# Kernel tuning notes

Hardware: AMD Instinct MI355X
Metric: run time of the kernel (lower is better)

## Reference

```python
import jax, jax.numpy as jnp
import numpy as np

DIM = 1024
NUM_HEADS = 16
SEQ_LEN = 4096


def setup_inputs() -> dict:
    key = jax.random.key(0)
    ks = jax.random.split(key, 9)
    s = DIM ** -0.5  # typical init scale for weights
    return {
        "x": jax.random.normal(ks[0], (SEQ_LEN, DIM), dtype=jnp.float32),
        "Wq": jax.random.normal(ks[1], (DIM, DIM), dtype=jnp.float32) * s,
        "bq": jax.random.normal(ks[2], (DIM,), dtype=jnp.float32) * s,
        "Wk": jax.random.normal(ks[3], (DIM, DIM), dtype=jnp.float32) * s,
        "bk": jax.random.normal(ks[4], (DIM,), dtype=jnp.float32) * s,
        "Wv": jax.random.normal(ks[5], (DIM, DIM), dtype=jnp.float32) * s,
        "bv": jax.random.normal(ks[6], (DIM,), dtype=jnp.float32) * s,
        "Wp": jax.random.normal(ks[7], (DIM, DIM), dtype=jnp.float32) * s,
        "bp": jax.random.normal(ks[8], (DIM,), dtype=jnp.float32) * s,
    }


def reference(x, Wq, bq, Wk, bk, Wv, bv, Wp, bp):
    T, C = x.shape
    H = NUM_HEADS
    Dh = C // H
    # QKV projections (eqx.nn.Linear: y = W @ x + b, vmapped over tokens)
    q = (x @ Wq.T + bq).reshape(T, H, Dh).swapaxes(0, 1)  # [H, T, Dh]
    k = (x @ Wk.T + bk).reshape(T, H, Dh).swapaxes(0, 1)
    v = (x @ Wv.T + bv).reshape(T, H, Dh).swapaxes(0, 1)
    # NOTE: original scales by C**-0.5 (full dim), not head_dim**-0.5
    attn = jnp.einsum("htd,hsd->hts", q, k) * (C ** -0.5)  # [H, T, T]
    causal = jnp.tril(jnp.ones((T, T), dtype=bool))[None, :, :]
    attn = jnp.where(causal, attn, -jnp.inf)
    attn = jax.nn.softmax(attn, axis=-1)
    out = jnp.einsum("hts,hsd->htd", attn, v)  # [H, T, Dh]
    out = out.swapaxes(0, 1).reshape(T, C)
    return out @ Wp.T + bp
```

## Files before the change

kernel.cpp:

```cpp
#include <hip/hip_runtime.h>
#include <stdint.h>

typedef unsigned short u16;
typedef __bf16 bf16x8 __attribute__((ext_vector_type(8)));
typedef u16 u16x8 __attribute__((ext_vector_type(8)));
typedef float f32x4 __attribute__((ext_vector_type(4)));
typedef float f32x16 __attribute__((ext_vector_type(16)));

#define SEQ 4096
#define CD 1024
#define NH 16
#define DHD 64

__device__ __forceinline__ u16 f2bf(float f) {
  union { float f; unsigned u; } v; v.f = f;
  unsigned r = v.u + 0x7fffu + ((v.u >> 16) & 1u);
  return (u16)(r >> 16);
}
__device__ __forceinline__ u16 f2bf_trunc(float f) {
  union { float f; unsigned u; } v; v.f = f;
  return (u16)(v.u >> 16);
}

__device__ __forceinline__ void load_lds16(const u16* g, u16* l) {
  __builtin_amdgcn_global_load_lds((const __attribute__((address_space(1))) void*)g,
                                   (__attribute__((address_space(3))) void*)l, 16, 0, 0);
}

__global__ __launch_bounds__(256) void cvt_all(const float* __restrict__ x, const float* __restrict__ Wq,
                                               const float* __restrict__ Wk, const float* __restrict__ Wv,
                                               const float* __restrict__ Wp,
                                               u16* __restrict__ xb, u16* __restrict__ Wb, u16* __restrict__ Wpb) {
  int b = blockIdx.x;
  const float* src; u16* dst; int base;
  if (b < 2048)      { src = x;  dst = xb;             base = b; }
  else if (b < 2560) { src = Wq; dst = Wb;             base = b - 2048; }
  else if (b < 3072) { src = Wk; dst = Wb + CD * CD;   base = b - 2560; }
  else if (b < 3584) { src = Wv; dst = Wb + 2*CD*CD;   base = b - 3072; }
  else               { src = Wp; dst = Wpb;            base = b - 3584; }
  int i = (base * 256 + (int)threadIdx.x) * 8;
  float4 a = *(const float4*)(src + i);
  float4 c = *(const float4*)(src + i + 4);
  u16x8 o;
  o[0] = f2bf(a.x); o[1] = f2bf(a.y); o[2] = f2bf(a.z); o[3] = f2bf(a.w);
  o[4] = f2bf(c.x); o[5] = f2bf(c.y); o[6] = f2bf(c.z); o[7] = f2bf(c.w);
  *(u16x8*)(dst + i) = o;
}

template<int MODE>
__device__ __forceinline__ void gemm_core(const u16* __restrict__ A, const u16* __restrict__ Bw,
                                          const float* __restrict__ bias, void* __restrict__ outp,
                                          float oscale) {
  constexpr int K = CD, N = CD;
  __shared__ u16 As[128 * 32];
  __shared__ u16 Bs[128 * 32];
  const int tid = threadIdx.x;
  const int w = tid >> 6, L = tid & 63, q = L >> 4, ln = L & 15;
  const int rowA0 = blockIdx.y * 128, rowB0 = blockIdx.x * 128;
  const int wr = (w >> 1) * 64, wc = (w & 1) * 64;
  f32x4 acc[4][4] = {};
  for (int k0 = 0; k0 < K; k0 += 32) {
#pragma unroll
    for (int pass = 0; pass < 2; ++pass) {
      int off = pass * 4096 + tid * 16;
      int row = off >> 6;
      int cole = (off & 63) >> 1;
      load_lds16(A + (size_t)(rowA0 + row) * K + k0 + cole, As + pass * 2048 + w * 512);
      load_lds16(Bw + (size_t)(rowB0 + row) * K + k0 + cole, Bs + pass * 2048 + w * 512);
    }
    __syncthreads();
    bf16x8 af[4], bg[4];
#pragma unroll
    for (int i = 0; i < 4; ++i) af[i] = *(const bf16x8*)(As + (wr + i * 16 + ln) * 32 + q * 8);
#pragma unroll
    for (int i = 0; i < 4; ++i) bg[i] = *(const bf16x8*)(Bs + (wc + i * 16 + ln) * 32 + q * 8);
#pragma unroll
    for (int i = 0; i < 4; ++i)
#pragma unroll
      for (int j = 0; j < 4; ++j)
        acc[i][j] = __builtin_amdgcn_mfma_f32_16x16x32_bf16(af[i], bg[j], acc[i][j], 0, 0, 0);
    __syncthreads();
  }
#pragma unroll
  for (int i = 0; i < 4; ++i) {
#pragma unroll
    for (int j = 0; j < 4; ++j) {
      int col = rowB0 + wc + j * 16 + ln;
      float bb = bias[col];
#pragma unroll
      for (int r = 0; r < 4; ++r) {
        int row = rowA0 + wr + i * 16 + q * 4 + r;
        float v = (acc[i][j][r] + bb) * oscale;
        if (MODE == 0)      ((u16*)outp)[(size_t)row * N + col] = f2bf(v);
        else if (MODE == 1) ((u16*)outp)[(size_t)col * SEQ + row] = f2bf(v);
        else                ((float*)outp)[(size_t)row * N + col] = v;
      }
    }
  }
}

__global__ __launch_bounds__(256) void gemm_qkv(const u16* __restrict__ A, const u16* __restrict__ W3,
                                                const float* __restrict__ bq, const float* __restrict__ bk,
                                                const float* __restrict__ bv, u16* __restrict__ Qb,
                                                u16* __restrict__ Kb, u16* __restrict__ VTb) {
  int z = blockIdx.z;
  if (z == 0)      gemm_core<0>(A, W3,              bq, Qb,  0.03125f);
  else if (z == 1) gemm_core<0>(A, W3 + CD * CD,    bk, Kb,  1.0f);
  else             gemm_core<1>(A, W3 + 2 * CD * CD, bv, VTb, 1.0f);
}

__global__ __launch_bounds__(256) void gemm_proj(const u16* __restrict__ A, const u16* __restrict__ Bw,
                                                 const float* __restrict__ bias, float* __restrict__ out) {
  gemm_core<2>(A, Bw, bias, out, 1.0f);
}

__global__ __launch_bounds__(256, 3) void attn_kernel(const u16* __restrict__ Q, const u16* __restrict__ Kg,
                                                      const u16* __restrict__ VTg, u16* __restrict__ O) {
  __shared__ u16 Ks[64 * 72];
  __shared__ u16 Vt[64 * 72];
  __shared__ u16 Ps[4 * 32 * 72];
  const int tid = threadIdx.x, w = tid >> 6, L = tid & 63;
  const int ln = L & 31, hh = L >> 5;
  const int b = blockIdx.x;
  const int qb = (SEQ / 128 - 1) - (b >> 4);
  const int h = b & 15;
  const int qbase = qb * 128;
  const int colH = h * DHD;
  const int qrow0 = qbase + w * 32;
  bf16x8 qf[4];
#pragma unroll
  for (int kk = 0; kk < 4; ++kk)
    qf[kk] = *(const bf16x8*)(Q + (size_t)(qrow0 + ln) * CD + colH + kk * 16 + hh * 8);
  f32x16 o_acc[2] = {};
  float lsum[16] = {};
  u16* Pw = Ps + w * 32 * 72;
  const int ntiles = 2 * qb + 2;
  const int row0 = tid >> 3, row1 = 32 + (tid >> 3), x0 = tid & 7;
  u16x8 kr[2], vr[2];
  kr[0] = *(const u16x8*)(Kg + (size_t)row0 * CD + colH + x0 * 8);
  kr[1] = *(const u16x8*)(Kg + (size_t)row1 * CD + colH + x0 * 8);
  vr[0] = *(const u16x8*)(VTg + (size_t)(colH + row0) * SEQ + x0 * 8);
  vr[1] = *(const u16x8*)(VTg + (size_t)(colH + row1) * SEQ + x0 * 8);
  for (int jt = 0; jt < ntiles; ++jt) {
    __syncthreads();
    *(u16x8*)(Ks + row0 * 72 + x0 * 8) = kr[0];
    *(u16x8*)(Ks + row1 * 72 + x0 * 8) = kr[1];
    *(u16x8*)(Vt + row0 * 72 + x0 * 8) = vr[0];
    *(u16x8*)(Vt + row1 * 72 + x0 * 8) = vr[1];
    __syncthreads();
    if (jt + 1 < ntiles) {
      size_t kb2 = (size_t)(jt + 1) * 64;
      kr[0] = *(const u16x8*)(Kg + (kb2 + row0) * CD + colH + x0 * 8);
      kr[1] = *(const u16x8*)(Kg + (kb2 + row1) * CD + colH + x0 * 8);
      vr[0] = *(const u16x8*)(VTg + (size_t)(colH + row0) * SEQ + kb2 + x0 * 8);
      vr[1] = *(const u16x8*)(VTg + (size_t)(colH + row1) * SEQ + kb2 + x0 * 8);
    }
    const int kbase = jt * 64;
    if (kbase <= qrow0 + 31) {
      const bool diag = (kbase + 63 > qrow0);
#pragma unroll
      for (int nt = 0; nt < 2; ++nt) {
        f32x16 acc = {};
#pragma unroll
        for (int kk = 0; kk < 4; ++kk) {
          bf16x8 kf = *(const bf16x8*)(Ks + (nt * 32 + ln) * 72 + kk * 16 + hh * 8);
          acc = __builtin_amdgcn_mfma_f32_32x32x16_bf16(qf[kk], kf, acc, 0, 0, 0);
        }
        const int kg = kbase + nt * 32 + ln;
#pragma unroll
        for (int r = 0; r < 16; ++r) {
          const int rrow = (r & 3) + 8 * (r >> 2) + 4 * hh;
          float sv = acc[r];
          if (diag && kg > qrow0 + rrow) sv = -1e30f;
          float p = __expf(sv);
          lsum[r] += p;
          Pw[rrow * 72 + nt * 32 + ln] = f2bf_trunc(p);
        }
      }
      asm volatile("s_waitcnt lgkmcnt(0)" ::: "memory");
      bf16x8 pf[4];
#pragma unroll
      for (int kk = 0; kk < 4; ++kk)
        pf[kk] = *(const bf16x8*)(Pw + ln * 72 + kk * 16 + hh * 8);
#pragma unroll
      for (int nt = 0; nt < 2; ++nt)
#pragma unroll
        for (int kk = 0; kk < 4; ++kk) {
          bf16x8 vf = *(const bf16x8*)(Vt + (nt * 32 + ln) * 72 + kk * 16 + hh * 8);
          o_acc[nt] = __builtin_amdgcn_mfma_f32_32x32x16_bf16(pf[kk], vf, o_acc[nt], 0, 0, 0);
        }
    }
  }
#pragma unroll
  for (int m = 1; m < 32; m <<= 1)
#pragma unroll
    for (int r = 0; r < 16; ++r) lsum[r] += __shfl_xor(lsum[r], m, 64);
  float inv[16];
#pragma unroll
  for (int r = 0; r < 16; ++r) inv[r] = 1.0f / lsum[r];
#pragma unroll
  for (int nt = 0; nt < 2; ++nt)
#pragma unroll
    for (int r = 0; r < 16; ++r) {
      const int rrow = (r & 3) + 8 * (r >> 2) + 4 * hh;
      const int row = qrow0 + rrow;
      const int col = colH + nt * 32 + ln;
      O[(size_t)row * CD + col] = f2bf(o_acc[nt][r] * inv[r]);
    }
}

extern "C" void kernel_launch(void* const* d_in, const int* in_sizes, int n_in,
                              void* d_out, int out_size, void* d_ws, size_t ws_size,
                              hipStream_t stream) {
  const float* x  = (const float*)d_in[0];
  const float* Wq = (const float*)d_in[1];
  const float* bq = (const float*)d_in[2];
  const float* Wk = (const float*)d_in[3];
  const float* bk = (const float*)d_in[4];
  const float* Wv = (const float*)d_in[5];
  const float* bv = (const float*)d_in[6];
  const float* Wp = (const float*)d_in[7];
  const float* bp = (const float*)d_in[8];

  char* ws = (char*)d_ws;
  u16* xb  = (u16*)(ws);
  u16* Wb  = (u16*)(ws + (8u << 20));
  u16* Wpb = (u16*)(ws + (14u << 20));
  u16* Qb  = (u16*)(ws + (16u << 20));
  u16* Kb  = (u16*)(ws + (24u << 20));
  u16* VTb = (u16*)(ws + (32u << 20));
  u16* Ab  = (u16*)(ws + (40u << 20));

  cvt_all<<<4096, 256, 0, stream>>>(x, Wq, Wk, Wv, Wp, xb, Wb, Wpb);
  gemm_qkv<<<dim3(CD / 128, SEQ / 128, 3), 256, 0, stream>>>(xb, Wb, bq, bk, bv, Qb, Kb, VTb);
  attn_kernel<<<(SEQ / 128) * NH, 256, 0, stream>>>(Qb, Kb, VTb, Ab);
  gemm_proj<<<dim3(CD / 128, SEQ / 128), 256, 0, stream>>>(Ab, Wpb, bp, (float*)d_out);
}
```

Baseline: 242.6 us.

## Keep attention probabilities in registers via transposed MFMA and permlane swap

Restructures the attention kernel to compute S^T (keys x queries), so each lane owns one query row. The P tile is then packed to bf16 in registers and redistributed with v_permlane32_swap rather than going through LDS. The block shrinks to 128 threads and 64 query rows, and K/V tiles are double-buffered so each iteration needs one barrier instead of two. Row sums collapse to a single scalar per lane, and outputs are written as 4-wide vectors. Smaller blocks double the grid but reduce K/V reuse per block, and the permlane instruction ties the code to newer CDNA targets.

```diff
diff --git a/kernel.cpp b/kernel.cpp
--- a/kernel.cpp
+++ b/kernel.cpp
@@ -4,6 +4,7 @@
 typedef unsigned short u16;
 typedef __bf16 bf16x8 __attribute__((ext_vector_type(8)));
 typedef u16 u16x8 __attribute__((ext_vector_type(8)));
+typedef u16 u16x4 __attribute__((ext_vector_type(4)));
 typedef float f32x4 __attribute__((ext_vector_type(4)));
 typedef float f32x16 __attribute__((ext_vector_type(16)));
 
@@ -17,9 +18,8 @@
   unsigned r = v.u + 0x7fffu + ((v.u >> 16) & 1u);
   return (u16)(r >> 16);
 }
-__device__ __forceinline__ u16 f2bf_trunc(float f) {
-  union { float f; unsigned u; } v; v.f = f;
-  return (u16)(v.u >> 16);
+__device__ __forceinline__ unsigned fbits(float f) {
+  union { float f; unsigned u; } v; v.f = f; return v.u;
 }
 
 __device__ __forceinline__ void load_lds16(const u16* g, u16* l) {
@@ -104,8 +104,8 @@
                                                 const float* __restrict__ bv, u16* __restrict__ Qb,
                                                 u16* __restrict__ Kb, u16* __restrict__ VTb) {
   int z = blockIdx.z;
-  if (z == 0)      gemm_core<0>(A, W3,              bq, Qb,  0.03125f);
-  else if (z == 1) gemm_core<0>(A, W3 + CD * CD,    bk, Kb,  1.0f);
+  if (z == 0)      gemm_core<0>(A, W3,               bq, Qb,  0.03125f);
+  else if (z == 1) gemm_core<0>(A, W3 + CD * CD,     bk, Kb,  1.0f);
   else             gemm_core<1>(A, W3 + 2 * CD * CD, bv, VTb, 1.0f);
 }
 
@@ -114,98 +114,99 @@
   gemm_core<2>(A, Bw, bias, out, 1.0f);
 }
 
-__global__ __launch_bounds__(256, 3) void attn_kernel(const u16* __restrict__ Q, const u16* __restrict__ Kg,
-                                                      const u16* __restrict__ VTg, u16* __restrict__ O) {
-  __shared__ u16 Ks[64 * 72];
-  __shared__ u16 Vt[64 * 72];
-  __shared__ u16 Ps[4 * 32 * 72];
+__global__ __launch_bounds__(128) void attn_kernel(const u16* __restrict__ Q, const u16* __restrict__ Kg,
+                                                   const u16* __restrict__ VTg, u16* __restrict__ O) {
+  __shared__ u16 Ks[2][64 * 72];
+  __shared__ u16 Vt[2][64 * 72];
   const int tid = threadIdx.x, w = tid >> 6, L = tid & 63;
   const int ln = L & 31, hh = L >> 5;
   const int b = blockIdx.x;
-  const int qb = (SEQ / 128 - 1) - (b >> 4);
+  const int qt = (SEQ / 64 - 1) - (b >> 4);
   const int h = b & 15;
-  const int qbase = qb * 128;
   const int colH = h * DHD;
-  const int qrow0 = qbase + w * 32;
+  const int qrow0 = qt * 64 + w * 32;
   bf16x8 qf[4];
 #pragma unroll
   for (int kk = 0; kk < 4; ++kk)
     qf[kk] = *(const bf16x8*)(Q + (size_t)(qrow0 + ln) * CD + colH + kk * 16 + hh * 8);
-  f32x16 o_acc[2] = {};
-  float lsum[16] = {};
-  u16* Pw = Ps + w * 32 * 72;
-  const int ntiles = 2 * qb + 2;
-  const int row0 = tid >> 3, row1 = 32 + (tid >> 3), x0 = tid & 7;
-  u16x8 kr[2], vr[2];
-  kr[0] = *(const u16x8*)(Kg + (size_t)row0 * CD + colH + x0 * 8);
-  kr[1] = *(const u16x8*)(Kg + (size_t)row1 * CD + colH + x0 * 8);
-  vr[0] = *(const u16x8*)(VTg + (size_t)(colH + row0) * SEQ + x0 * 8);
-  vr[1] = *(const u16x8*)(VTg + (size_t)(colH + row1) * SEQ + x0 * 8);
-  for (int jt = 0; jt < ntiles; ++jt) {
+  f32x16 oa[2] = {};
+  float lsum = 0.f;
+  const int srow = tid >> 3, sx = tid & 7;
+  u16x8 kr[4], vr[4];
+#pragma unroll
+  for (int p = 0; p < 4; ++p) {
+    kr[p] = *(const u16x8*)(Kg + (size_t)(p * 16 + srow) * CD + colH + sx * 8);
+    vr[p] = *(const u16x8*)(VTg + (size_t)(colH + p * 16 + srow) * SEQ + sx * 8);
+  }
+  for (int jt = 0; jt <= qt; ++jt) {
+    const int buf = jt & 1;
+    u16* KsB = Ks[buf];
+    u16* VtB = Vt[buf];
+#pragma unroll
+    for (int p = 0; p < 4; ++p) {
+      *(u16x8*)(KsB + (p * 16 + srow) * 72 + sx * 8) = kr[p];
+      *(u16x8*)(VtB + (p * 16 + srow) * 72 + sx * 8) = vr[p];
+    }
     __syncthreads();
-    *(u16x8*)(Ks + row0 * 72 + x0 * 8) = kr[0];
-    *(u16x8*)(Ks + row1 * 72 + x0 * 8) = kr[1];
-    *(u16x8*)(Vt + row0 * 72 + x0 * 8) = vr[0];
-    *(u16x8*)(Vt + row1 * 72 + x0 * 8) = vr[1];
-    __syncthreads();
-    if (jt + 1 < ntiles) {
-      size_t kb2 = (size_t)(jt + 1) * 64;
-      kr[0] = *(const u16x8*)(Kg + (kb2 + row0) * CD + colH + x0 * 8);
-      kr[1] = *(const u16x8*)(Kg + (kb2 + row1) * CD + colH + x0 * 8);
-      vr[0] = *(const u16x8*)(VTg + (size_t)(colH + row0) * SEQ + kb2 + x0 * 8);
-      vr[1] = *(const u16x8*)(VTg + (size_t)(colH + row1) * SEQ + kb2 + x0 * 8);
-    }
-    const int kbase = jt * 64;
-    if (kbase <= qrow0 + 31) {
-      const bool diag = (kbase + 63 > qrow0);
-#pragma unroll
-      for (int nt = 0; nt < 2; ++nt) {
-        f32x16 acc = {};
-#pragma unroll
-        for (int kk = 0; kk < 4; ++kk) {
-          bf16x8 kf = *(const bf16x8*)(Ks + (nt * 32 + ln) * 72 + kk * 16 + hh * 8);
-          acc = __builtin_amdgcn_mfma_f32_32x32x16_bf16(qf[kk], kf, acc, 0, 0, 0);
+    if (jt < qt) {
+      const size_t kb2 = (size_t)(jt + 1) * 64;
+#pragma unroll
+      for (int p = 0; p < 4; ++p) {
+        kr[p] = *(const u16x8*)(Kg + (kb2 + p * 16 + srow) * CD + colH + sx * 8);
+        vr[p] = *(const u16x8*)(VTg + (size_t)(colH + p * 16 + srow) * SEQ + kb2 + sx * 8);
+      }
+    }
+    const bool diag = (jt == qt);
+    unsigned pk[16];
+#pragma unroll
+    for (int nt = 0; nt < 2; ++nt) {
+      f32x16 a = {};
+#pragma unroll
+      for (int kk = 0; kk < 4; ++kk) {
+        bf16x8 kf = *(const bf16x8*)(KsB + (nt * 32 + ln) * 72 + kk * 16 + hh * 8);
+        a = __builtin_amdgcn_mfma_f32_32x32x16_bf16(kf, qf[kk], a, 0, 0, 0);
+      }
+#pragma unroll
+      for (int r = 0; r < 16; ++r) {
+        float sv = a[r];
+        if (diag) {
+          const int key_l = nt * 32 + (r & 3) + 8 * (r >> 2) + 4 * hh;
+          if (key_l > w * 32 + ln) sv = -1e30f;
         }
-        const int kg = kbase + nt * 32 + ln;
-#pragma unroll
-        for (int r = 0; r < 16; ++r) {
-          const int rrow = (r & 3) + 8 * (r >> 2) + 4 * hh;
-          float sv = acc[r];
-          if (diag && kg > qrow0 + rrow) sv = -1e30f;
-          float p = __expf(sv);
-          lsum[r] += p;
-          Pw[rrow * 72 + nt * 32 + ln] = f2bf_trunc(p);
-        }
-      }
-      asm volatile("s_waitcnt lgkmcnt(0)" ::: "memory");
-      bf16x8 pf[4];
-#pragma unroll
-      for (int kk = 0; kk < 4; ++kk)
-        pf[kk] = *(const bf16x8*)(Pw + ln * 72 + kk * 16 + hh * 8);
-#pragma unroll
-      for (int nt = 0; nt < 2; ++nt)
-#pragma unroll
-        for (int kk = 0; kk < 4; ++kk) {
-          bf16x8 vf = *(const bf16x8*)(Vt + (nt * 32 + ln) * 72 + kk * 16 + hh * 8);
-          o_acc[nt] = __builtin_amdgcn_mfma_f32_32x32x16_bf16(pf[kk], vf, o_acc[nt], 0, 0, 0);
-        }
-    }
-  }
-#pragma unroll
-  for (int m = 1; m < 32; m <<= 1)
-#pragma unroll
-    for (int r = 0; r < 16; ++r) lsum[r] += __shfl_xor(lsum[r], m, 64);
-  float inv[16];
-#pragma unroll
-  for (int r = 0; r < 16; ++r) inv[r] = 1.0f / lsum[r];
-#pragma unroll
-  for (int nt = 0; nt < 2; ++nt)
-#pragma unroll
-    for (int r = 0; r < 16; ++r) {
-      const int rrow = (r & 3) + 8 * (r >> 2) + 4 * hh;
-      const int row = qrow0 + rrow;
-      const int col = colH + nt * 32 + ln;
-      O[(size_t)row * CD + col] = f2bf(o_acc[nt][r] * inv[r]);
+        float p = __expf(sv);
+        lsum += p;
+        a[r] = p;
+      }
+#pragma unroll
+      for (int i = 0; i < 8; ++i)
+        pk[nt * 8 + i] = __builtin_amdgcn_perm(fbits(a[2 * i + 1]), fbits(a[2 * i]), 0x07060302);
+    }
+#pragma unroll
+    for (int b0 = 0; b0 < 16; b0 += 4) {
+      asm("v_permlane32_swap_b32 %0, %1" : "+v"(pk[b0 + 0]), "+v"(pk[b0 + 2]));
+      asm("v_permlane32_swap_b32 %0, %1" : "+v"(pk[b0 + 1]), "+v"(pk[b0 + 3]));
+    }
+#pragma unroll
+    for (int g = 0; g < 2; ++g)
+#pragma unroll
+      for (int s = 0; s < 4; ++s) {
+        bf16x8 vf = *(const bf16x8*)(VtB + (g * 32 + ln) * 72 + s * 16 + hh * 8);
+        union { unsigned u[4]; bf16x8 v; } pf;
+        pf.u[0] = pk[s * 4 + 0]; pf.u[1] = pk[s * 4 + 1];
+        pf.u[2] = pk[s * 4 + 2]; pf.u[3] = pk[s * 4 + 3];
+        oa[g] = __builtin_amdgcn_mfma_f32_32x32x16_bf16(vf, pf.v, oa[g], 0, 0, 0);
+      }
+  }
+  lsum += __shfl_xor(lsum, 32, 64);
+  const float inv = 1.0f / lsum;
+#pragma unroll
+  for (int g = 0; g < 2; ++g)
+#pragma unroll
+    for (int rg = 0; rg < 4; ++rg) {
+      u16x4 ov;
+#pragma unroll
+      for (int i = 0; i < 4; ++i) ov[i] = f2bf(oa[g][rg * 4 + i] * inv);
+      *(u16x4*)(O + (size_t)(qrow0 + ln) * CD + colH + g * 32 + 8 * rg + 4 * hh) = ov;
     }
 }
 
@@ -233,6 +234,6 @@
 
   cvt_all<<<4096, 256, 0, stream>>>(x, Wq, Wk, Wv, Wp, xb, Wb, Wpb);
   gemm_qkv<<<dim3(CD / 128, SEQ / 128, 3), 256, 0, stream>>>(xb, Wb, bq, bk, bv, Qb, Kb, VTb);
-  attn_kernel<<<(SEQ / 128) * NH, 256, 0, stream>>>(Qb, Kb, VTb, Ab);
+  attn_kernel<<<(SEQ / 64) * NH, 128, 0, stream>>>(Qb, Kb, VTb, Ab);
   gemm_proj<<<dim3(CD / 128, SEQ / 128), 256, 0, stream>>>(Ab, Wpb, bp, (float*)d_out);
 }
```

Result: faster. 222.7 us (-8.2%).
